# Optimization experiments

Measured on AMD Instinct MI355X. Metric: run time of the kernel, lower is better.

## Reference

```python
import jax, jax.numpy as jnp
import numpy as np

N = 50000
E = 1600000
D = 128
BN_EPS = 1e-5


def setup_inputs() -> dict:
    key = jax.random.key(0)
    ks = jax.random.split(key, 6)
    feature = jax.random.normal(ks[0], (N, D), dtype=jnp.float32)
    snorm_n = jax.random.uniform(ks[1], (N, 1), dtype=jnp.float32)
    src = jax.random.randint(ks[2], (E,), 0, N, dtype=jnp.int64)
    dst = jax.random.randint(ks[3], (E,), 0, N, dtype=jnp.int64)
    W = jax.random.normal(ks[4], (D, D), dtype=jnp.float32) * (1.0 / np.sqrt(D))
    b = jax.random.normal(ks[5], (D,), dtype=jnp.float32) * 0.01
    gamma = jnp.ones((D,), dtype=jnp.float32)
    beta = jnp.zeros((D,), dtype=jnp.float32)
    return {"feature": feature, "snorm_n": snorm_n, "src": src, "dst": dst,
            "W": W, "b": b, "gamma": gamma, "beta": beta}


def reference(feature, snorm_n, src, dst, W, b, gamma, beta):
    # --- copy_src + mean reduce (DGL update_all) ---
    msg = feature[src]                                    # [E, D] gather
    agg = jax.ops.segment_sum(msg, dst, num_segments=N)   # [N, D] scatter-add
    deg = jax.ops.segment_sum(jnp.ones((src.shape[0],), feature.dtype), dst,
                              num_segments=N)             # [N]
    has_msg = deg > 0
    mean = agg / jnp.maximum(deg, 1.0)[:, None]
    # nodes with no incoming edges keep their original 'h' (DGL semantics)
    h = jnp.where(has_msg[:, None], mean, feature)
    # --- apply_nodes: linear ---
    h = h @ W.T + b
    # --- graph norm ---
    h = h * snorm_n
    # --- batch norm (training-mode stats, biased variance, eps=1e-5) ---
    mu = jnp.mean(h, axis=0)
    var = jnp.mean((h - mu) ** 2, axis=0)
    h = (h - mu) / jnp.sqrt(var + BN_EPS) * gamma + beta
    # --- activation + residual (dropout p=0 -> identity) ---
    h = jax.nn.relu(h)
    h = feature + h
    return h
```

## Files before the change

### kernel.cpp

```cpp
#include <hip/hip_runtime.h>

#define D 128
#define BN_EPS 1e-5f
#define ROWS 16
#define CHUNK 4096
#define CAP_SCAN 512

typedef unsigned int u32;
typedef unsigned short u16;

__device__ inline u32 pk_bf16(float x, float y) {
    u32 ux = __float_as_uint(x), uy = __float_as_uint(y);
    ux = (ux + 0x7fffu + ((ux >> 16) & 1u)) >> 16;
    uy = (uy + 0x7fffu + ((uy >> 16) & 1u)) >> 16;
    return ux | (uy << 16);
}

__global__ __launch_bounds__(256) void cast_transpose(const float* __restrict__ feat,
                                                      u16* __restrict__ feat16,
                                                      const float* __restrict__ W,
                                                      float* __restrict__ Wt,
                                                      int ncast) {
    int b = blockIdx.x;
    if (b < ncast) {
        size_t i = ((size_t)b * 256 + threadIdx.x) * 8;
        float4 f0 = *reinterpret_cast<const float4*>(feat + i);
        float4 f1 = *reinterpret_cast<const float4*>(feat + i + 4);
        uint4 o;
        o.x = pk_bf16(f0.x, f0.y);
        o.y = pk_bf16(f0.z, f0.w);
        o.z = pk_bf16(f1.x, f1.y);
        o.w = pk_bf16(f1.z, f1.w);
        *reinterpret_cast<uint4*>(feat16 + i) = o;
    } else {
        int i = (b - ncast) * 256 + threadIdx.x;
        int r = i >> 7, c = i & 127;
        Wt[c * D + r] = W[i];
    }
}

__global__ __launch_bounds__(256) void passA(const int* __restrict__ dst,
                                             int* __restrict__ blkcnt,
                                             int nch, int nedges) {
    __shared__ int cnt[256];
    cnt[threadIdx.x] = 0;
    __syncthreads();
    const int e0 = blockIdx.x * CHUNK;
    for (int r = 0; r < CHUNK / 256; ++r) {
        int e = e0 + r * 256 + threadIdx.x;
        if (e < nedges) atomicAdd(&cnt[dst[e] >> 8], 1);
    }
    __syncthreads();
    blkcnt[(size_t)threadIdx.x * nch + blockIdx.x] = cnt[threadIdx.x];
}

__global__ __launch_bounds__(CAP_SCAN) void scanB1(int* __restrict__ blkcnt,
                                                   int* __restrict__ gtot,
                                                   int nch) {
    __shared__ int s[CAP_SCAN];
    const int t = threadIdx.x;
    const size_t row = (size_t)blockIdx.x * nch;
    int v = (t < nch) ? blkcnt[row + t] : 0;
    s[t] = v;
    __syncthreads();
    for (int off = 1; off < CAP_SCAN; off <<= 1) {
        int u = (t >= off) ? s[t - off] : 0;
        __syncthreads();
        s[t] += u;
        __syncthreads();
    }
    if (t < nch) blkcnt[row + t] = s[t] - v;
    if (t == 0) gtot[blockIdx.x] = s[CAP_SCAN - 1];
}

__global__ __launch_bounds__(256) void scanB2(const int* __restrict__ gtot,
                                              int* __restrict__ bucket_base,
                                              int* __restrict__ bucket_cnt) {
    __shared__ int s[256];
    const int t = threadIdx.x;
    int v = gtot[t];
    s[t] = v;
    __syncthreads();
    for (int off = 1; off < 256; off <<= 1) {
        int u = (t >= off) ? s[t - off] : 0;
        __syncthreads();
        s[t] += u;
        __syncthreads();
    }
    bucket_base[t] = s[t] - v;
    bucket_cnt[t] = v;
}

__global__ __launch_bounds__(256) void passB(const int* __restrict__ src,
                                             const int* __restrict__ dst,
                                             const int* __restrict__ blkcnt,
                                             const int* __restrict__ bucket_base,
                                             u32* __restrict__ gpacked,
                                             int nch, int nedges) {
    __shared__ int cnt[256];
    __shared__ int gbase[256];
    const int t = threadIdx.x;
    gbase[t] = blkcnt[(size_t)t * nch + blockIdx.x] + bucket_base[t];
    cnt[t] = 0;
    __syncthreads();
    const int e0 = blockIdx.x * CHUNK;
    for (int r = 0; r < CHUNK / 256; ++r) {
        int e = e0 + r * 256 + t;
        if (e < nedges) {
            int d = dst[e];
            int b = d >> 8;
            int pos = atomicAdd(&cnt[b], 1);
            gpacked[gbase[b] + pos] = (u32)src[e] | ((u32)(d & 255) << 16);
        }
    }
}

__global__ __launch_bounds__(256) void pass2(const u32* __restrict__ gpacked,
                                             const int* __restrict__ bucket_base,
                                             const int* __restrict__ bucket_cnt,
                                             u16* __restrict__ epos,
                                             int* __restrict__ count,
                                             int* __restrict__ offs,
                                             int nnodes) {
    __shared__ int cnt[256], lo[256], cur[256];
    const int t = threadIdx.x;
    const int b = blockIdx.x;
    const int nE = bucket_cnt[b];
    const int base = bucket_base[b];
    cnt[t] = 0;
    __syncthreads();
    for (int i = t; i < nE; i += 256) atomicAdd(&cnt[gpacked[base + i] >> 16], 1);
    __syncthreads();
    int v = cnt[t];
    lo[t] = v;
    __syncthreads();
    for (int off = 1; off < 256; off <<= 1) {
        int u = (t >= off) ? lo[t - off] : 0;
        __syncthreads();
        lo[t] += u;
        __syncthreads();
    }
    int excl = lo[t] - v;
    int n = (b << 8) + t;
    if (n < nnodes) { count[n] = v; offs[n] = base + excl; }
    cur[t] = excl;
    __syncthreads();
    for (int i = t; i < nE; i += 256) {
        u32 p = gpacked[base + i];
        int pos = atomicAdd(&cur[p >> 16], 1);
        epos[base + pos] = (u16)(p & 0xffffu);
    }
}

__global__ __launch_bounds__(256, 6) void fused_agg_linear(
        const float* __restrict__ feat,
        const u16* __restrict__ feat16,
        const float* __restrict__ snorm,
        const int* __restrict__ offs,
        const int* __restrict__ count,
        const u16* __restrict__ epos,
        const float* __restrict__ Wt,
        const float* __restrict__ bias,
        float* __restrict__ y,
        float* __restrict__ partial) {
    __shared__ float hs[ROWS][D];
    const int row0 = blockIdx.x * ROWS;
    const int wid = threadIdx.x >> 6;
    const int lane = threadIdx.x & 63;
    const int q = lane >> 4;
    const int ql = lane & 15;

#define LDB(s) (*reinterpret_cast<const uint4*>(feat16 + (size_t)(s) * D + 8 * ql))
#define ADD8(a, u) { \
    a[0] += __uint_as_float((u).x << 16); a[1] += __uint_as_float((u).x & 0xffff0000u); \
    a[2] += __uint_as_float((u).y << 16); a[3] += __uint_as_float((u).y & 0xffff0000u); \
    a[4] += __uint_as_float((u).z << 16); a[5] += __uint_as_float((u).z & 0xffff0000u); \
    a[6] += __uint_as_float((u).w << 16); a[7] += __uint_as_float((u).w & 0xffff0000u); }

    for (int rr = 0; rr < 4; ++rr) {
        const int r = wid * 4 + rr;
        const int n = row0 + r;
        const int dg = count[n];
        const int o = offs[n];
        float a0[8], a1[8];
        #pragma unroll
        for (int k = 0; k < 8; ++k) { a0[k] = 0.0f; a1[k] = 0.0f; }

        for (int base = 0; base < dg; base += 64) {
            const int m = min(64, dg - base);
            int myidx = (lane < m) ? (int)epos[o + base + lane] : 0;
            int j = 0;
            for (; j + 8 <= m; j += 8) {
                int s0 = __shfl(myidx, j + q, 64);
                int s1 = __shfl(myidx, j + 4 + q, 64);
                uint4 u0 = LDB(s0);
                uint4 u1 = LDB(s1);
                ADD8(a0, u0);
                ADD8(a1, u1);
            }
            if (j + 4 <= m) {
                int s0 = __shfl(myidx, j + q, 64);
                uint4 u0 = LDB(s0);
                ADD8(a0, u0);
                j += 4;
            }
            int rem = m - j;
            if (rem) {
                int s0 = __shfl(myidx, j + (q < rem ? q : 0), 64);
                if (q < rem) { uint4 u0 = LDB(s0); ADD8(a1, u0); }
            }
        }

        float av[8];
        #pragma unroll
        for (int k = 0; k < 8; ++k) {
            float v = a0[k] + a1[k];
            v += __shfl_xor(v, 16, 64);
            v += __shfl_xor(v, 32, 64);
            av[k] = v;
        }
        if (dg > 0) {
            float inv = 1.0f / (float)dg;
            #pragma unroll
            for (int k = 0; k < 8; ++k) av[k] *= inv;
        } else {
            float4 f0 = *reinterpret_cast<const float4*>(feat + (size_t)n * D + 8 * ql);
            float4 f1 = *reinterpret_cast<const float4*>(feat + (size_t)n * D + 8 * ql + 4);
            av[0] = f0.x; av[1] = f0.y; av[2] = f0.z; av[3] = f0.w;
            av[4] = f1.x; av[5] = f1.y; av[6] = f1.z; av[7] = f1.w;
        }
        if (q == 0) {
            *reinterpret_cast<float4*>(&hs[r][8 * ql]) = make_float4(av[0], av[1], av[2], av[3]);
            *reinterpret_cast<float4*>(&hs[r][8 * ql + 4]) = make_float4(av[4], av[5], av[6], av[7]);
        }
    }
#undef LDB
#undef ADD8
    __syncthreads();

    const int d = threadIdx.x & 127;
    const int half2 = threadIdx.x >> 7;
    float acc[8];
    #pragma unroll
    for (int r = 0; r < 8; ++r) acc[r] = 0.0f;

    for (int k = 0; k < D; k += 4) {
        float w0 = Wt[(k + 0) * D + d];
        float w1 = Wt[(k + 1) * D + d];
        float w2 = Wt[(k + 2) * D + d];
        float w3 = Wt[(k + 3) * D + d];
        #pragma unroll
        for (int r = 0; r < 8; ++r) {
            float4 h4 = *reinterpret_cast<const float4*>(&hs[half2 * 8 + r][k]);
            acc[r] += h4.x * w0 + h4.y * w1 + h4.z * w2 + h4.w * w3;
        }
    }

    const float bb = bias[d];
    float psum = 0.0f, psq = 0.0f;
    #pragma unroll
    for (int r = 0; r < 8; ++r) {
        const int n = row0 + half2 * 8 + r;
        float v = (acc[r] + bb) * snorm[n];
        y[(size_t)n * D + d] = v;
        psum += v;
        psq += v * v;
    }
    __syncthreads();
    if (half2 == 1) { hs[0][d] = psum; hs[1][d] = psq; }
    __syncthreads();
    if (half2 == 0) {
        psum += hs[0][d];
        psq += hs[1][d];
        partial[(size_t)blockIdx.x * 256 + d] = psum;
        partial[(size_t)blockIdx.x * 256 + 128 + d] = psq;
    }
}

__global__ __launch_bounds__(256) void bn_reduce(const float* __restrict__ partial,
                                                 const float* __restrict__ gamma,
                                                 const float* __restrict__ beta,
                                                 float* __restrict__ bnparam,
                                                 int nchunk, float inv_n) {
    const int d = blockIdx.x;
    float s = 0.0f, q = 0.0f;
    for (int b = threadIdx.x; b < nchunk; b += 256) {
        s += partial[(size_t)b * 256 + d];
        q += partial[(size_t)b * 256 + 128 + d];
    }
    for (int off = 32; off > 0; off >>= 1) {
        s += __shfl_down(s, off, 64);
        q += __shfl_down(q, off, 64);
    }
    __shared__ float ss[4], qq[4];
    int wid = threadIdx.x >> 6;
    int lane = threadIdx.x & 63;
    if (lane == 0) { ss[wid] = s; qq[wid] = q; }
    __syncthreads();
    if (threadIdx.x == 0) {
        float S = ss[0] + ss[1] + ss[2] + ss[3];
        float Q = qq[0] + qq[1] + qq[2] + qq[3];
        float mu = S * inv_n;
        float var = Q * inv_n - mu * mu;
        var = fmaxf(var, 0.0f);
        float rstd = rsqrtf(var + BN_EPS);
        float scale = gamma[d] * rstd;
        float shift = beta[d] - mu * scale;
        bnparam[d] = scale;
        bnparam[D + d] = shift;
    }
}

__global__ __launch_bounds__(256) void finalize(const float* __restrict__ feat,
                                                float* __restrict__ y,
                                                const float* __restrict__ bnparam,
                                                int total4) {
    int i = blockIdx.x * 256 + threadIdx.x;
    if (i >= total4) return;
    int c = i & 31;
    float4 v = reinterpret_cast<float4*>(y)[i];
    float4 f = reinterpret_cast<const float4*>(feat)[i];
    float4 sc = reinterpret_cast<const float4*>(bnparam)[c];
    float4 sh = reinterpret_cast<const float4*>(bnparam + D)[c];
    v.x = f.x + fmaxf(v.x * sc.x + sh.x, 0.0f);
    v.y = f.y + fmaxf(v.y * sc.y + sh.y, 0.0f);
    v.z = f.z + fmaxf(v.z * sc.z + sh.z, 0.0f);
    v.w = f.w + fmaxf(v.w * sc.w + sh.w, 0.0f);
    reinterpret_cast<float4*>(y)[i] = v;
}

extern "C" void kernel_launch(void* const* d_in, const int* in_sizes, int n_in,
                              void* d_out, int out_size, void* d_ws, size_t ws_size,
                              hipStream_t stream) {
    const float* feat  = (const float*)d_in[0];
    const float* snorm = (const float*)d_in[1];
    const int*   src   = (const int*)d_in[2];
    const int*   dst   = (const int*)d_in[3];
    const float* W     = (const float*)d_in[4];
    const float* bias  = (const float*)d_in[5];
    const float* gamma = (const float*)d_in[6];
    const float* beta  = (const float*)d_in[7];

    const int N = in_sizes[1];
    const int E = in_sizes[2];
    const int nblk = N / ROWS;
    const int nch = (E + CHUNK - 1) / CHUNK;
    const int nbuck = (N + 255) >> 8;
    const int ncast = (N * D) / (8 * 256);

    int* count       = (int*)d_ws;
    int* offs        = count + N;
    int* blkcnt      = offs + N;
    int* gtot        = blkcnt + (size_t)256 * nch;
    int* bucket_base = gtot + 256;
    int* bucket_cnt  = bucket_base + 256;
    u32* gpacked     = (u32*)(bucket_cnt + 256);
    u16* epos        = (u16*)(gpacked + E);
    u16* feat16      = epos + E;
    float* Wt        = (float*)(feat16 + (size_t)N * D);
    float* partial   = Wt + D * D;
    float* bnparam   = partial + (size_t)nblk * 256;

    float* y = (float*)d_out;

    cast_transpose<<<ncast + 64, 256, 0, stream>>>(feat, feat16, W, Wt, ncast);

    passA<<<nch, 256, 0, stream>>>(dst, blkcnt, nch, E);
    scanB1<<<256, CAP_SCAN, 0, stream>>>(blkcnt, gtot, nch);
    scanB2<<<1, 256, 0, stream>>>(gtot, bucket_base, bucket_cnt);
    passB<<<nch, 256, 0, stream>>>(src, dst, blkcnt, bucket_base, gpacked, nch, E);
    pass2<<<nbuck, 256, 0, stream>>>(gpacked, bucket_base, bucket_cnt,
                                     epos, count, offs, N);

    fused_agg_linear<<<nblk, 256, 0, stream>>>(feat, feat16, snorm, offs, count,
                                               epos, Wt, bias, y, partial);

    bn_reduce<<<D, 256, 0, stream>>>(partial, gamma, beta, bnparam,
                                     nblk, 1.0f / (float)N);

    {
        int total4 = N * D / 4;
        finalize<<<(total4 + 255) / 256, 256, 0, stream>>>(feat, y, bnparam, total4);
    }
}
```

Before: 159.1 us.

## Merge prep kernels, fuse two-level scan via last-block counter, widen blocks

Folds the cast/transpose and the per-chunk destination histogram into one launch. The two scan kernels become one, where the last block to finish (found with an atomic counter and release/acquire ordering) does the bucket-level scan. pass2 and the fused aggregation/linear kernel move to 512-thread blocks, so each wave handles fewer rows and more waves share each tile. This cuts kernel launches and serial tail phases, at the cost of atomic synchronization overhead and different occupancy and register tradeoffs.

```diff
diff --git a/kernel.cpp b/kernel.cpp
--- a/kernel.cpp
+++ b/kernel.cpp
@@ -16,12 +16,16 @@
     return ux | (uy << 16);
 }
 
-__global__ __launch_bounds__(256) void cast_transpose(const float* __restrict__ feat,
-                                                      u16* __restrict__ feat16,
-                                                      const float* __restrict__ W,
-                                                      float* __restrict__ Wt,
-                                                      int ncast) {
-    int b = blockIdx.x;
+__global__ __launch_bounds__(256) void prep(const float* __restrict__ feat,
+                                            u16* __restrict__ feat16,
+                                            const float* __restrict__ W,
+                                            float* __restrict__ Wt,
+                                            const int* __restrict__ dst,
+                                            int* __restrict__ blkcnt,
+                                            int* __restrict__ sync_counter,
+                                            int ncast, int nch, int nedges) {
+    __shared__ int cnt[256];
+    const int b = blockIdx.x;
     if (b < ncast) {
         size_t i = ((size_t)b * 256 + threadIdx.x) * 8;
         float4 f0 = *reinterpret_cast<const float4*>(feat + i);
@@ -32,32 +36,33 @@
         o.z = pk_bf16(f1.x, f1.y);
         o.w = pk_bf16(f1.z, f1.w);
         *reinterpret_cast<uint4*>(feat16 + i) = o;
-    } else {
+    } else if (b < ncast + 64) {
         int i = (b - ncast) * 256 + threadIdx.x;
         int r = i >> 7, c = i & 127;
         Wt[c * D + r] = W[i];
-    }
-}
-
-__global__ __launch_bounds__(256) void passA(const int* __restrict__ dst,
-                                             int* __restrict__ blkcnt,
-                                             int nch, int nedges) {
-    __shared__ int cnt[256];
-    cnt[threadIdx.x] = 0;
-    __syncthreads();
-    const int e0 = blockIdx.x * CHUNK;
-    for (int r = 0; r < CHUNK / 256; ++r) {
-        int e = e0 + r * 256 + threadIdx.x;
-        if (e < nedges) atomicAdd(&cnt[dst[e] >> 8], 1);
-    }
-    __syncthreads();
-    blkcnt[(size_t)threadIdx.x * nch + blockIdx.x] = cnt[threadIdx.x];
-}
-
-__global__ __launch_bounds__(CAP_SCAN) void scanB1(int* __restrict__ blkcnt,
-                                                   int* __restrict__ gtot,
-                                                   int nch) {
+        if (i == 0) *sync_counter = 0;
+    } else {
+        const int c = b - ncast - 64;
+        cnt[threadIdx.x] = 0;
+        __syncthreads();
+        const int e0 = c * CHUNK;
+        for (int r = 0; r < CHUNK / 256; ++r) {
+            int e = e0 + r * 256 + threadIdx.x;
+            if (e < nedges) atomicAdd(&cnt[dst[e] >> 8], 1);
+        }
+        __syncthreads();
+        blkcnt[(size_t)threadIdx.x * nch + c] = cnt[threadIdx.x];
+    }
+}
+
+__global__ __launch_bounds__(CAP_SCAN) void scanB(int* __restrict__ blkcnt,
+                                                  int* __restrict__ gtot,
+                                                  int* __restrict__ bucket_base,
+                                                  int* __restrict__ bucket_cnt,
+                                                  int* __restrict__ sync_counter,
+                                                  int nch) {
     __shared__ int s[CAP_SCAN];
+    __shared__ int lastflag;
     const int t = threadIdx.x;
     const size_t row = (size_t)blockIdx.x * nch;
     int v = (t < nch) ? blkcnt[row + t] : 0;
@@ -70,25 +75,27 @@
         __syncthreads();
     }
     if (t < nch) blkcnt[row + t] = s[t] - v;
-    if (t == 0) gtot[blockIdx.x] = s[CAP_SCAN - 1];
-}
-
-__global__ __launch_bounds__(256) void scanB2(const int* __restrict__ gtot,
-                                              int* __restrict__ bucket_base,
-                                              int* __restrict__ bucket_cnt) {
-    __shared__ int s[256];
-    const int t = threadIdx.x;
-    int v = gtot[t];
-    s[t] = v;
-    __syncthreads();
-    for (int off = 1; off < 256; off <<= 1) {
-        int u = (t >= off) ? s[t - off] : 0;
-        __syncthreads();
-        s[t] += u;
-        __syncthreads();
-    }
-    bucket_base[t] = s[t] - v;
-    bucket_cnt[t] = v;
+    if (t == 0) {
+        __hip_atomic_store(&gtot[blockIdx.x], s[CAP_SCAN - 1],
+                           __ATOMIC_RELEASE, __HIP_MEMORY_SCOPE_AGENT);
+        int old = __hip_atomic_fetch_add(sync_counter, 1,
+                                         __ATOMIC_ACQ_REL, __HIP_MEMORY_SCOPE_AGENT);
+        lastflag = (old == 255);
+    }
+    __syncthreads();
+    if (lastflag) {
+        int g = (t < 256) ? __hip_atomic_load(&gtot[t], __ATOMIC_ACQUIRE,
+                                              __HIP_MEMORY_SCOPE_AGENT) : 0;
+        s[t] = g;
+        __syncthreads();
+        for (int off = 1; off < 256; off <<= 1) {
+            int u = (t >= off && t < 256) ? s[t - off] : 0;
+            __syncthreads();
+            if (t < 256) s[t] += u;
+            __syncthreads();
+        }
+        if (t < 256) { bucket_base[t] = s[t] - g; bucket_cnt[t] = g; }
+    }
 }
 
 __global__ __launch_bounds__(256) void passB(const int* __restrict__ src,
@@ -115,7 +122,7 @@
     }
 }
 
-__global__ __launch_bounds__(256) void pass2(const u32* __restrict__ gpacked,
+__global__ __launch_bounds__(512) void pass2(const u32* __restrict__ gpacked,
                                              const int* __restrict__ bucket_base,
                                              const int* __restrict__ bucket_cnt,
                                              u16* __restrict__ epos,
@@ -127,32 +134,34 @@
     const int b = blockIdx.x;
     const int nE = bucket_cnt[b];
     const int base = bucket_base[b];
-    cnt[t] = 0;
-    __syncthreads();
-    for (int i = t; i < nE; i += 256) atomicAdd(&cnt[gpacked[base + i] >> 16], 1);
-    __syncthreads();
-    int v = cnt[t];
-    lo[t] = v;
+    if (t < 256) cnt[t] = 0;
+    __syncthreads();
+    for (int i = t; i < nE; i += 512) atomicAdd(&cnt[gpacked[base + i] >> 16], 1);
+    __syncthreads();
+    int v = (t < 256) ? cnt[t] : 0;
+    if (t < 256) lo[t] = v;
     __syncthreads();
     for (int off = 1; off < 256; off <<= 1) {
-        int u = (t >= off) ? lo[t - off] : 0;
-        __syncthreads();
-        lo[t] += u;
-        __syncthreads();
-    }
-    int excl = lo[t] - v;
-    int n = (b << 8) + t;
-    if (n < nnodes) { count[n] = v; offs[n] = base + excl; }
-    cur[t] = excl;
-    __syncthreads();
-    for (int i = t; i < nE; i += 256) {
+        int u = (t >= off && t < 256) ? lo[t - off] : 0;
+        __syncthreads();
+        if (t < 256) lo[t] += u;
+        __syncthreads();
+    }
+    if (t < 256) {
+        int excl = lo[t] - v;
+        int n = (b << 8) + t;
+        if (n < nnodes) { count[n] = v; offs[n] = base + excl; }
+        cur[t] = excl;
+    }
+    __syncthreads();
+    for (int i = t; i < nE; i += 512) {
         u32 p = gpacked[base + i];
         int pos = atomicAdd(&cur[p >> 16], 1);
         epos[base + pos] = (u16)(p & 0xffffu);
     }
 }
 
-__global__ __launch_bounds__(256, 6) void fused_agg_linear(
+__global__ __launch_bounds__(512, 4) void fused_agg_linear(
         const float* __restrict__ feat,
         const u16* __restrict__ feat16,
         const float* __restrict__ snorm,
@@ -177,8 +186,8 @@
     a[4] += __uint_as_float((u).z << 16); a[5] += __uint_as_float((u).z & 0xffff0000u); \
     a[6] += __uint_as_float((u).w << 16); a[7] += __uint_as_float((u).w & 0xffff0000u); }
 
-    for (int rr = 0; rr < 4; ++rr) {
-        const int r = wid * 4 + rr;
+    for (int rr = 0; rr < 2; ++rr) {
+        const int r = wid * 2 + rr;
         const int n = row0 + r;
         const int dg = count[n];
         const int o = offs[n];
@@ -239,10 +248,10 @@
     __syncthreads();
 
     const int d = threadIdx.x & 127;
-    const int half2 = threadIdx.x >> 7;
-    float acc[8];
+    const int g = threadIdx.x >> 7;
+    float acc[4];
     #pragma unroll
-    for (int r = 0; r < 8; ++r) acc[r] = 0.0f;
+    for (int r = 0; r < 4; ++r) acc[r] = 0.0f;
 
     for (int k = 0; k < D; k += 4) {
         float w0 = Wt[(k + 0) * D + d];
@@ -250,8 +259,8 @@
         float w2 = Wt[(k + 2) * D + d];
         float w3 = Wt[(k + 3) * D + d];
         #pragma unroll
-        for (int r = 0; r < 8; ++r) {
-            float4 h4 = *reinterpret_cast<const float4*>(&hs[half2 * 8 + r][k]);
+        for (int r = 0; r < 4; ++r) {
+            float4 h4 = *reinterpret_cast<const float4*>(&hs[g * 4 + r][k]);
             acc[r] += h4.x * w0 + h4.y * w1 + h4.z * w2 + h4.w * w3;
         }
     }
@@ -259,19 +268,19 @@
     const float bb = bias[d];
     float psum = 0.0f, psq = 0.0f;
     #pragma unroll
-    for (int r = 0; r < 8; ++r) {
-        const int n = row0 + half2 * 8 + r;
+    for (int r = 0; r < 4; ++r) {
+        const int n = row0 + g * 4 + r;
         float v = (acc[r] + bb) * snorm[n];
         y[(size_t)n * D + d] = v;
         psum += v;
         psq += v * v;
     }
     __syncthreads();
-    if (half2 == 1) { hs[0][d] = psum; hs[1][d] = psq; }
-    __syncthreads();
-    if (half2 == 0) {
-        psum += hs[0][d];
-        psq += hs[1][d];
+    if (g > 0) { hs[2 * (g - 1)][d] = psum; hs[2 * (g - 1) + 1][d] = psq; }
+    __syncthreads();
+    if (g == 0) {
+        psum += hs[0][d] + hs[2][d] + hs[4][d];
+        psq  += hs[1][d] + hs[3][d] + hs[5][d];
         partial[(size_t)blockIdx.x * 256 + d] = psum;
         partial[(size_t)blockIdx.x * 256 + 128 + d] = psq;
     }
@@ -354,7 +363,8 @@
     int* gtot        = blkcnt + (size_t)256 * nch;
     int* bucket_base = gtot + 256;
     int* bucket_cnt  = bucket_base + 256;
-    u32* gpacked     = (u32*)(bucket_cnt + 256);
+    int* sync_counter= bucket_cnt + 256;
+    u32* gpacked     = (u32*)(sync_counter + 4);
     u16* epos        = (u16*)(gpacked + E);
     u16* feat16      = epos + E;
     float* Wt        = (float*)(feat16 + (size_t)N * D);
@@ -363,16 +373,19 @@
 
     float* y = (float*)d_out;
 
-    cast_transpose<<<ncast + 64, 256, 0, stream>>>(feat, feat16, W, Wt, ncast);
-
-    passA<<<nch, 256, 0, stream>>>(dst, blkcnt, nch, E);
-    scanB1<<<256, CAP_SCAN, 0, stream>>>(blkcnt, gtot, nch);
-    scanB2<<<1, 256, 0, stream>>>(gtot, bucket_base, bucket_cnt);
+    prep<<<ncast + 64 + nch, 256, 0, stream>>>(feat, feat16, W, Wt, dst,
+                                               blkcnt, sync_counter,
+                                               ncast, nch, E);
+
+    scanB<<<256, CAP_SCAN, 0, stream>>>(blkcnt, gtot, bucket_base, bucket_cnt,
+                                        sync_counter, nch);
+
     passB<<<nch, 256, 0, stream>>>(src, dst, blkcnt, bucket_base, gpacked, nch, E);
-    pass2<<<nbuck, 256, 0, stream>>>(gpacked, bucket_base, bucket_cnt,
+
+    pass2<<<nbuck, 512, 0, stream>>>(gpacked, bucket_base, bucket_cnt,
                                      epos, count, offs, N);
 
-    fused_agg_linear<<<nblk, 256, 0, stream>>>(feat, feat16, snorm, offs, count,
+    fused_agg_linear<<<nblk, 512, 0, stream>>>(feat, feat16, snorm, offs, count,
                                                epos, Wt, bias, y, partial);
 
     bn_reduce<<<D, 256, 0, stream>>>(partial, gamma, beta, bnparam,
```

New measurement: 163.9 us. +3.0%, slower.
